# Performance work log

Measured on AMD Instinct MI355X. Metric: run time of the kernel, lower is better.

Reference implementation:

```python
import jax, jax.numpy as jnp
import numpy as np


def setup_inputs() -> dict:
    key = jax.random.key(0)
    ks = jax.random.split(key, 5)
    B, C, H, W = 4, 64, 64, 64
    C8 = C // 8
    return {
        "x_opt": jax.random.normal(ks[0], (B, C, H, W), jnp.float32),
        "x_sar": jax.random.normal(ks[1], (B, C, H, W), jnp.float32),
        "wq": jax.random.normal(ks[2], (C8, C), jnp.float32) * 0.05,
        "bq": jnp.zeros((C8,), jnp.float32),
        "wk": jax.random.normal(ks[3], (C8, C), jnp.float32) * 0.05,
        "bk": jnp.zeros((C8,), jnp.float32),
        "wv": jax.random.normal(ks[4], (C, C), jnp.float32) * 0.05,
        "bv": jnp.zeros((C,), jnp.float32),
        "gamma": jnp.zeros((1,), jnp.float32),
    }


def reference(x_opt, x_sar, wq, bq, wk, bk, wv, bv, gamma):
    b, c, h, w = x_opt.shape
    n = h * w
    xo = x_opt.reshape(b, c, n)  # [b, c, N]
    xs = x_sar.reshape(b, c, n)
    # 1x1 convs == channel matmuls
    q = jnp.einsum('oc,bcn->bon', wq, xo) + bq[None, :, None]  # [b, c//8, N]
    k = jnp.einsum('oc,bcn->bon', wk, xs) + bk[None, :, None]  # [b, c//8, N]
    v = jnp.einsum('oc,bcn->bon', wv, xs) + bv[None, :, None]  # [b, c, N]
    # attn[b, n, m] = softmax_m( q[:, :, n] . k[:, :, m] )  -- NO 1/sqrt(d) scaling
    scores = jnp.einsum('bdn,bdm->bnm', q, k)  # [b, N, N]
    attn = jax.nn.softmax(scores, axis=-1)
    # out[b, c, n] = sum_m v[b, c, m] * attn[b, n, m]
    out = jnp.einsum('bcm,bnm->bcn', v, attn).reshape(b, c, h, w)
    return gamma[0] * out + x_opt
```

## Files before the change

### kernel.cpp

```cpp
#include <hip/hip_runtime.h>
#include <hip/hip_bf16.h>
#include <stdint.h>

#define NDIM 4096
#define CDIM 64
#define NSPLIT 8
#define SPAN (NDIM / NSPLIT)
#define LOG2E 1.44269504088896f

typedef float f32x16 __attribute__((ext_vector_type(16)));
typedef short bf16x8 __attribute__((ext_vector_type(8)));
union U4B { uint4 u; bf16x8 b; };

static __device__ __forceinline__ uint32_t cvtpk(float lo, float hi) {
  uint32_t r;
  asm("v_cvt_pk_bf16_f32 %0, %1, %2" : "=v"(r) : "v"(lo), "v"(hi));
  return r;
}
static __device__ __forceinline__ uint16_t f2bf(float f) {
  uint32_t r;
  asm("v_cvt_pk_bf16_f32 %0, %1, %1" : "=v"(r) : "v"(f));
  return (uint16_t)r;
}
static __device__ __forceinline__ float fexp2(float x) {
  return __builtin_amdgcn_exp2f(x);
}

__global__ __launch_bounds__(256) void proj_kernel(
    const float* __restrict__ x_opt, const float* __restrict__ x_sar,
    const float* __restrict__ wq, const float* __restrict__ bq,
    const float* __restrict__ wk, const float* __restrict__ bk,
    const float* __restrict__ wvp, const float* __restrict__ bv,
    uint16_t* __restrict__ qf, uint16_t* __restrict__ kfp,
    uint16_t* __restrict__ vf2)
{
  const int tid = threadIdx.x;
  const int w = tid >> 6;
  const int l = tid & 63;
  const int x = l & 31;
  const int hi = l >> 5;

  const int id = blockIdx.x;
  const int b = id >> 7;
  const int n0 = (id & 127) * 32;
  const size_t xbase = (size_t)b * CDIM * NDIM;

  const float* xsrc = (w == 2) ? x_opt : x_sar;
  bf16x8 xB[4];
#pragma unroll
  for (int kc = 0; kc < 4; kc++) {
    float sv[8];
#pragma unroll
    for (int j = 0; j < 8; j++)
      sv[j] = xsrc[xbase + (size_t)(kc * 16 + hi * 8 + j) * NDIM + n0 + x];
    U4B us;
    us.u = make_uint4(cvtpk(sv[0], sv[1]), cvtpk(sv[2], sv[3]),
                      cvtpk(sv[4], sv[5]), cvtpk(sv[6], sv[7]));
    xB[kc] = us.b;
  }

  bf16x8 aF[4];
#pragma unroll
  for (int kc = 0; kc < 4; kc++) {
    U4B ua;
    ua.u = make_uint4(0u, 0u, 0u, 0u);
    if (w < 2) {
      const float* wr = wvp + (w * 32 + x) * 64 + kc * 16 + hi * 8;
      float4 wa = ((const float4*)wr)[0];
      float4 wb = ((const float4*)wr)[1];
      ua.u = make_uint4(cvtpk(wa.x, wa.y), cvtpk(wa.z, wa.w),
                        cvtpk(wb.x, wb.y), cvtpk(wb.z, wb.w));
    } else if (x < 8) {
      const float* wr = ((w == 2) ? wq : wk) + x * 64 + kc * 16 + hi * 8;
      float4 wa = ((const float4*)wr)[0];
      float4 wb = ((const float4*)wr)[1];
      ua.u = make_uint4(cvtpk(wa.x, wa.y), cvtpk(wa.z, wa.w),
                        cvtpk(wb.x, wb.y), cvtpk(wb.z, wb.w));
    }
    aF[kc] = ua.b;
  }

  const f32x16 z16 = {0.f,0.f,0.f,0.f, 0.f,0.f,0.f,0.f,
                      0.f,0.f,0.f,0.f, 0.f,0.f,0.f,0.f};
  f32x16 acc = z16;
#pragma unroll
  for (int kc = 0; kc < 4; kc++)
    acc = __builtin_amdgcn_mfma_f32_32x32x16_bf16(aF[kc], xB[kc], acc, 0, 0, 0);

  if (w < 2) {
    const size_t kbbase = (size_t)b * 256 + (n0 >> 4) + (x >> 4);
    const int kk = x & 15;
#pragma unroll
    for (int r = 0; r < 16; r++) {
      const int row = w * 32 + (r & 3) + 8 * (r >> 2) + 4 * hi;
      vf2[(kbbase * 64 + row) * 16 + kk] = f2bf(acc[r] + bv[row]);
    }
  } else if (w == 2) {
    float gv[4];
#pragma unroll
    for (int r = 0; r < 4; r++) gv[r] = (acc[r] + bq[4 * hi + r]) * LOG2E;
    const size_t nrow = ((size_t)b * NDIM + n0 + x) * 16;
    uint2 st;
    st.x = cvtpk(gv[0], gv[1]); st.y = cvtpk(gv[2], gv[3]);
    *(uint2*)(qf + nrow + hi * 4) = st;
    if (hi == 0) {
      const uint4 z4 = make_uint4(0u, 0u, 0u, 0u);
      *(uint4*)(qf + nrow + 8) = z4;
    }
  } else {
    float gv[4];
#pragma unroll
    for (int r = 0; r < 4; r++) gv[r] = acc[r] + bk[4 * hi + r];
    uint2 st;
    st.x = cvtpk(gv[0], gv[1]); st.y = cvtpk(gv[2], gv[3]);
    *(uint2*)(kfp + ((size_t)b * NDIM + n0 + x) * 8 + hi * 4) = st;
  }
}

__global__ __launch_bounds__(256, 4) void attn_kernel(
    const uint16_t* __restrict__ qf, const uint16_t* __restrict__ kfp,
    const uint16_t* __restrict__ vf2,
    uint16_t* __restrict__ po, float* __restrict__ ls)
{
  const int tid = threadIdx.x;
  const int w = tid >> 6;
  const int l = tid & 63;
  const int x = l & 31;
  const int hi = l >> 5;

  const int id = blockIdx.x;
  const int sp = id & 7;
  const int qb = (id >> 3) & 31;
  const int b = id >> 8;

  const int n0 = qb * 128;
  const int qrow = n0 + w * 32 + x;

  U4B qfr;
  qfr.u = *(const uint4*)(qf + ((size_t)b * NDIM + qrow) * 16 + hi * 8);

  const uint32_t hmask = hi ? 0u : 0xFFFFFFFFu;

  const uint16_t* kbase = kfp + ((size_t)b * NDIM + sp * SPAN + x) * 8;
  const uint16_t* vbase =
      vf2 + (((size_t)b * 256 + sp * 32) * 64 + x) * 16 + hi * 8;

  const f32x16 z16 = {0.f,0.f,0.f,0.f, 0.f,0.f,0.f,0.f,
                      0.f,0.f,0.f,0.f, 0.f,0.f,0.f,0.f};
  f32x16 oacc0 = z16, oacc1 = z16;
  float lacc[4] = {0.f, 0.f, 0.f, 0.f};

  uint4 kc   = *(const uint4*)(kbase);
  uint4 va00 = *(const uint4*)(vbase);
  uint4 va01 = *(const uint4*)(vbase + 512);
  uint4 va10 = *(const uint4*)(vbase + 1024);
  uint4 va11 = *(const uint4*)(vbase + 1536);

#pragma unroll
  for (int gq = 0; gq < 16; gq++) {
    const int vo = (gq + 1) * 2048;
    uint4 kn   = *(const uint4*)(kbase + (gq + 1) * 256);
    uint4 vn00 = *(const uint4*)(vbase + vo);
    uint4 vn01 = *(const uint4*)(vbase + vo + 512);
    uint4 vn10 = *(const uint4*)(vbase + vo + 1024);
    uint4 vn11 = *(const uint4*)(vbase + vo + 1536);

    U4B ka;
    ka.u.x = kc.x & hmask; ka.u.y = kc.y & hmask;
    ka.u.z = kc.z & hmask; ka.u.w = kc.w & hmask;
    f32x16 s = __builtin_amdgcn_mfma_f32_32x32x16_bf16(ka.b, qfr.b, z16, 0, 0, 0);

    uint32_t W[8];
#pragma unroll
    for (int j = 0; j < 8; j++) {
      const float p0 = fexp2(s[2 * j]);
      const float p1 = fexp2(s[2 * j + 1]);
      W[j] = cvtpk(p0, p1);
      lacc[j & 3] += p0 + p1;
    }

    __builtin_amdgcn_s_setprio(1);
    {
      uint32_t a0 = W[0], b0 = W[2], a1 = W[1], b1 = W[3];
      asm("v_permlane32_swap_b32 %0, %1" : "+v"(a0), "+v"(b0));
      asm("v_permlane32_swap_b32 %0, %1" : "+v"(a1), "+v"(b1));
      U4B pf, va, vb;
      pf.u = make_uint4(a0, a1, b0, b1);
      va.u = va00; vb.u = va01;
      oacc0 = __builtin_amdgcn_mfma_f32_32x32x16_bf16(va.b, pf.b, oacc0, 0, 0, 0);
      oacc1 = __builtin_amdgcn_mfma_f32_32x32x16_bf16(vb.b, pf.b, oacc1, 0, 0, 0);
    }
    {
      uint32_t a0 = W[4], b0 = W[6], a1 = W[5], b1 = W[7];
      asm("v_permlane32_swap_b32 %0, %1" : "+v"(a0), "+v"(b0));
      asm("v_permlane32_swap_b32 %0, %1" : "+v"(a1), "+v"(b1));
      U4B pf, va, vb;
      pf.u = make_uint4(a0, a1, b0, b1);
      va.u = va10; vb.u = va11;
      oacc0 = __builtin_amdgcn_mfma_f32_32x32x16_bf16(va.b, pf.b, oacc0, 0, 0, 0);
      oacc1 = __builtin_amdgcn_mfma_f32_32x32x16_bf16(vb.b, pf.b, oacc1, 0, 0, 0);
    }
    __builtin_amdgcn_s_setprio(0);

    __builtin_amdgcn_s_barrier();

    kc = kn; va00 = vn00; va01 = vn01; va10 = vn10; va11 = vn11;
  }

  uint16_t* prow = po + (((size_t)sp * 4 + b) * NDIM + qrow) * CDIM;
#pragma unroll
  for (int cb = 0; cb < 2; cb++) {
    const f32x16 oa = (cb == 0) ? oacc0 : oacc1;
#pragma unroll
    for (int u = 0; u < 4; u++) {
      uint2 st;
      st.x = cvtpk(oa[u * 4 + 0], oa[u * 4 + 1]);
      st.y = cvtpk(oa[u * 4 + 2], oa[u * 4 + 3]);
      *(uint2*)(prow + cb * 32 + u * 8 + hi * 4) = st;
    }
  }
  float ltot = (lacc[0] + lacc[1]) + (lacc[2] + lacc[3]);
  ltot += __shfl_xor(ltot, 32);
  if (hi == 0)
    ls[((size_t)sp * 4 + b) * NDIM + qrow] = ltot;
}

__global__ __launch_bounds__(256) void merge_kernel(
    const uint16_t* __restrict__ po, const float* __restrict__ ls,
    const float* __restrict__ x_opt, const float* __restrict__ gamma,
    float* __restrict__ out)
{
  __shared__ float ot[32][65];
  const int tid = threadIdx.x;
  const int b = blockIdx.x >> 7;
  const int n0 = (blockIdx.x & 127) * 32;
  {
    const int q = tid >> 3;
    const int co = (tid & 7) * 8;
    const int nq = n0 + q;
    float wsum = 0.f;
    float acc[8] = {0.f, 0.f, 0.f, 0.f, 0.f, 0.f, 0.f, 0.f};
#pragma unroll
    for (int s = 0; s < NSPLIT; s++) {
      wsum += ls[((size_t)s * 4 + b) * NDIM + nq];
      const uint4 pv = *(const uint4*)(po + (((size_t)s * 4 + b) * NDIM + nq) * CDIM + co);
      const uint32_t* pw = (const uint32_t*)&pv;
#pragma unroll
      for (int j = 0; j < 4; j++) {
        acc[j * 2 + 0] += __uint_as_float(pw[j] << 16);
        acc[j * 2 + 1] += __uint_as_float(pw[j] & 0xFFFF0000u);
      }
    }
    const float inv = 1.f / wsum;
#pragma unroll
    for (int j = 0; j < 8; j++) ot[q][co + j] = acc[j] * inv;
  }
  __syncthreads();
  {
    const float gm = gamma[0];
    const int c = tid >> 2;
    const int j8 = (tid & 3) * 8;
    const float* xp = x_opt + ((size_t)b * CDIM + c) * NDIM + n0 + j8;
    float* op = out + ((size_t)b * CDIM + c) * NDIM + n0 + j8;
#pragma unroll
    for (int h = 0; h < 2; h++) {
      float4 xv = ((const float4*)xp)[h];
      float4 ov;
      ov.x = gm * ot[j8 + h * 4 + 0][c] + xv.x;
      ov.y = gm * ot[j8 + h * 4 + 1][c] + xv.y;
      ov.z = gm * ot[j8 + h * 4 + 2][c] + xv.z;
      ov.w = gm * ot[j8 + h * 4 + 3][c] + xv.w;
      ((float4*)op)[h] = ov;
    }
  }
}

extern "C" void kernel_launch(void* const* d_in, const int* in_sizes, int n_in,
                              void* d_out, int out_size, void* d_ws, size_t ws_size,
                              hipStream_t stream) {
  const float* x_opt = (const float*)d_in[0];
  const float* x_sar = (const float*)d_in[1];
  const float* wq    = (const float*)d_in[2];
  const float* bq    = (const float*)d_in[3];
  const float* wk    = (const float*)d_in[4];
  const float* bk    = (const float*)d_in[5];
  const float* wvp   = (const float*)d_in[6];
  const float* bv    = (const float*)d_in[7];
  const float* gamma = (const float*)d_in[8];
  float* outp = (float*)d_out;

  uint16_t* qf  = (uint16_t*)d_ws;
  uint16_t* kfp = (uint16_t*)((char*)d_ws + 524288);
  uint16_t* vf2 = (uint16_t*)((char*)d_ws + 1048576);
  uint16_t* po  = (uint16_t*)((char*)d_ws + 3145728);
  float* lsp    = (float*)((char*)d_ws + 19922944);

  proj_kernel<<<512, 256, 0, stream>>>(x_opt, x_sar, wq, bq, wk, bk, wvp, bv,
                                       qf, kfp, vf2);
  attn_kernel<<<1024, 256, 0, stream>>>(qf, kfp, vf2, po, lsp);
  merge_kernel<<<512, 256, 0, stream>>>(po, lsp, x_opt, gamma, outp);
}
```

Baseline: 38.66 us.

## Process two query tiles per wave to reuse K/V loads, drop barrier

Each wave now handles 64 query rows (two 32-row MFMA tiles) instead of 32, so every loaded K and V fragment feeds twice as many MFMAs. This halves global/L2 traffic per unit of work and halves the grid to 512 blocks. The per-iteration workgroup barrier is removed and launch bounds drop to 2 waves/SIMD because of doubled accumulator registers. The risks are lower occupancy, less latency hiding, and fewer blocks (512) to fill 256 CUs.

New measurement: 54.93 us. 1.42x slower.

```diff
diff --git a/kernel.cpp b/kernel.cpp
--- a/kernel.cpp
+++ b/kernel.cpp
@@ -117,7 +117,7 @@
   }
 }
 
-__global__ __launch_bounds__(256, 4) void attn_kernel(
+__global__ __launch_bounds__(256, 2) void attn_kernel(
     const uint16_t* __restrict__ qf, const uint16_t* __restrict__ kfp,
     const uint16_t* __restrict__ vf2,
     uint16_t* __restrict__ po, float* __restrict__ ls)
@@ -130,14 +130,15 @@
 
   const int id = blockIdx.x;
   const int sp = id & 7;
-  const int qb = (id >> 3) & 31;
-  const int b = id >> 8;
-
-  const int n0 = qb * 128;
-  const int qrow = n0 + w * 32 + x;
-
-  U4B qfr;
-  qfr.u = *(const uint4*)(qf + ((size_t)b * NDIM + qrow) * 16 + hi * 8);
+  const int qb = (id >> 3) & 15;
+  const int b = id >> 7;
+
+  const int n0 = qb * 256;
+  const int qrow0 = n0 + w * 64 + x;
+
+  U4B qfr0, qfr1;
+  qfr0.u = *(const uint4*)(qf + ((size_t)b * NDIM + qrow0) * 16 + hi * 8);
+  qfr1.u = *(const uint4*)(qf + ((size_t)b * NDIM + qrow0 + 32) * 16 + hi * 8);
 
   const uint32_t hmask = hi ? 0u : 0xFFFFFFFFu;
 
@@ -147,8 +148,10 @@
 
   const f32x16 z16 = {0.f,0.f,0.f,0.f, 0.f,0.f,0.f,0.f,
                       0.f,0.f,0.f,0.f, 0.f,0.f,0.f,0.f};
-  f32x16 oacc0 = z16, oacc1 = z16;
-  float lacc[4] = {0.f, 0.f, 0.f, 0.f};
+  f32x16 oacc00 = z16, oacc01 = z16;
+  f32x16 oacc10 = z16, oacc11 = z16;
+  float lacc0[4] = {0.f, 0.f, 0.f, 0.f};
+  float lacc1[4] = {0.f, 0.f, 0.f, 0.f};
 
   uint4 kc   = *(const uint4*)(kbase);
   uint4 va00 = *(const uint4*)(vbase);
@@ -168,61 +171,82 @@
     U4B ka;
     ka.u.x = kc.x & hmask; ka.u.y = kc.y & hmask;
     ka.u.z = kc.z & hmask; ka.u.w = kc.w & hmask;
-    f32x16 s = __builtin_amdgcn_mfma_f32_32x32x16_bf16(ka.b, qfr.b, z16, 0, 0, 0);
-
-    uint32_t W[8];
+    f32x16 s0 = __builtin_amdgcn_mfma_f32_32x32x16_bf16(ka.b, qfr0.b, z16, 0, 0, 0);
+    f32x16 s1 = __builtin_amdgcn_mfma_f32_32x32x16_bf16(ka.b, qfr1.b, z16, 0, 0, 0);
+
+    uint32_t W0[8], W1[8];
 #pragma unroll
     for (int j = 0; j < 8; j++) {
-      const float p0 = fexp2(s[2 * j]);
-      const float p1 = fexp2(s[2 * j + 1]);
-      W[j] = cvtpk(p0, p1);
-      lacc[j & 3] += p0 + p1;
+      const float a0 = fexp2(s0[2 * j]);
+      const float a1 = fexp2(s0[2 * j + 1]);
+      W0[j] = cvtpk(a0, a1);
+      lacc0[j & 3] += a0 + a1;
+      const float c0 = fexp2(s1[2 * j]);
+      const float c1 = fexp2(s1[2 * j + 1]);
+      W1[j] = cvtpk(c0, c1);
+      lacc1[j & 3] += c0 + c1;
     }
 
     __builtin_amdgcn_s_setprio(1);
     {
-      uint32_t a0 = W[0], b0 = W[2], a1 = W[1], b1 = W[3];
+      uint32_t a0 = W0[0], b0 = W0[2], a1 = W0[1], b1 = W0[3];
+      uint32_t c0 = W1[0], d0 = W1[2], c1 = W1[1], d1 = W1[3];
       asm("v_permlane32_swap_b32 %0, %1" : "+v"(a0), "+v"(b0));
       asm("v_permlane32_swap_b32 %0, %1" : "+v"(a1), "+v"(b1));
-      U4B pf, va, vb;
-      pf.u = make_uint4(a0, a1, b0, b1);
+      asm("v_permlane32_swap_b32 %0, %1" : "+v"(c0), "+v"(d0));
+      asm("v_permlane32_swap_b32 %0, %1" : "+v"(c1), "+v"(d1));
+      U4B pf0, pf1, va, vb;
+      pf0.u = make_uint4(a0, a1, b0, b1);
+      pf1.u = make_uint4(c0, c1, d0, d1);
       va.u = va00; vb.u = va01;
-      oacc0 = __builtin_amdgcn_mfma_f32_32x32x16_bf16(va.b, pf.b, oacc0, 0, 0, 0);
-      oacc1 = __builtin_amdgcn_mfma_f32_32x32x16_bf16(vb.b, pf.b, oacc1, 0, 0, 0);
+      oacc00 = __builtin_amdgcn_mfma_f32_32x32x16_bf16(va.b, pf0.b, oacc00, 0, 0, 0);
+      oacc01 = __builtin_amdgcn_mfma_f32_32x32x16_bf16(vb.b, pf0.b, oacc01, 0, 0, 0);
+      oacc10 = __builtin_amdgcn_mfma_f32_32x32x16_bf16(va.b, pf1.b, oacc10, 0, 0, 0);
+      oacc11 = __builtin_amdgcn_mfma_f32_32x32x16_bf16(vb.b, pf1.b, oacc11, 0, 0, 0);
     }
     {
-      uint32_t a0 = W[4], b0 = W[6], a1 = W[5], b1 = W[7];
+      uint32_t a0 = W0[4], b0 = W0[6], a1 = W0[5], b1 = W0[7];
+      uint32_t c0 = W1[4], d0 = W1[6], c1 = W1[5], d1 = W1[7];
       asm("v_permlane32_swap_b32 %0, %1" : "+v"(a0), "+v"(b0));
       asm("v_permlane32_swap_b32 %0, %1" : "+v"(a1), "+v"(b1));
-      U4B pf, va, vb;
-      pf.u = make_uint4(a0, a1, b0, b1);
+      asm("v_permlane32_swap_b32 %0, %1" : "+v"(c0), "+v"(d0));
+      asm("v_permlane32_swap_b32 %0, %1" : "+v"(c1), "+v"(d1));
+      U4B pf0, pf1, va, vb;
+      pf0.u = make_uint4(a0, a1, b0, b1);
+      pf1.u = make_uint4(c0, c1, d0, d1);
       va.u = va10; vb.u = va11;
-      oacc0 = __builtin_amdgcn_mfma_f32_32x32x16_bf16(va.b, pf.b, oacc0, 0, 0, 0);
-      oacc1 = __builtin_amdgcn_mfma_f32_32x32x16_bf16(vb.b, pf.b, oacc1, 0, 0, 0);
+      oacc00 = __builtin_amdgcn_mfma_f32_32x32x16_bf16(va.b, pf0.b, oacc00, 0, 0, 0);
+      oacc01 = __builtin_amdgcn_mfma_f32_32x32x16_bf16(vb.b, pf0.b, oacc01, 0, 0, 0);
+      oacc10 = __builtin_amdgcn_mfma_f32_32x32x16_bf16(va.b, pf1.b, oacc10, 0, 0, 0);
+      oacc11 = __builtin_amdgcn_mfma_f32_32x32x16_bf16(vb.b, pf1.b, oacc11, 0, 0, 0);
     }
     __builtin_amdgcn_s_setprio(0);
 
-    __builtin_amdgcn_s_barrier();
-
     kc = kn; va00 = vn00; va01 = vn01; va10 = vn10; va11 = vn11;
   }
 
-  uint16_t* prow = po + (((size_t)sp * 4 + b) * NDIM + qrow) * CDIM;
-#pragma unroll
-  for (int cb = 0; cb < 2; cb++) {
-    const f32x16 oa = (cb == 0) ? oacc0 : oacc1;
-#pragma unroll
-    for (int u = 0; u < 4; u++) {
-      uint2 st;
-      st.x = cvtpk(oa[u * 4 + 0], oa[u * 4 + 1]);
-      st.y = cvtpk(oa[u * 4 + 2], oa[u * 4 + 3]);
-      *(uint2*)(prow + cb * 32 + u * 8 + hi * 4) = st;
-    }
-  }
-  float ltot = (lacc[0] + lacc[1]) + (lacc[2] + lacc[3]);
-  ltot += __shfl_xor(ltot, 32);
-  if (hi == 0)
-    ls[((size_t)sp * 4 + b) * NDIM + qrow] = ltot;
+#pragma unroll
+  for (int f = 0; f < 2; f++) {
+    const int qrow = qrow0 + f * 32;
+    uint16_t* prow = po + (((size_t)sp * 4 + b) * NDIM + qrow) * CDIM;
+#pragma unroll
+    for (int cb = 0; cb < 2; cb++) {
+      const f32x16 oa = (f == 0) ? (cb == 0 ? oacc00 : oacc01)
+                                 : (cb == 0 ? oacc10 : oacc11);
+#pragma unroll
+      for (int u = 0; u < 4; u++) {
+        uint2 st;
+        st.x = cvtpk(oa[u * 4 + 0], oa[u * 4 + 1]);
+        st.y = cvtpk(oa[u * 4 + 2], oa[u * 4 + 3]);
+        *(uint2*)(prow + cb * 32 + u * 8 + hi * 4) = st;
+      }
+    }
+    float ltot = (f == 0) ? (lacc0[0] + lacc0[1]) + (lacc0[2] + lacc0[3])
+                          : (lacc1[0] + lacc1[1]) + (lacc1[2] + lacc1[3]);
+    ltot += __shfl_xor(ltot, 32);
+    if (hi == 0)
+      ls[((size_t)sp * 4 + b) * NDIM + qrow] = ltot;
+  }
 }
 
 __global__ __launch_bounds__(256) void merge_kernel(
@@ -297,6 +321,6 @@
 
   proj_kernel<<<512, 256, 0, stream>>>(x_opt, x_sar, wq, bq, wk, bk, wvp, bv,
                                        qf, kfp, vf2);
-  attn_kernel<<<1024, 256, 0, stream>>>(qf, kfp, vf2, po, lsp);
+  attn_kernel<<<512, 256, 0, stream>>>(qf, kfp, vf2, po, lsp);
   merge_kernel<<<512, 256, 0, stream>>>(po, lsp, x_opt, gamma, outp);
 }
```

## Store attention partials channel-major and simplify merge without LDS transpose

Applied to the files above, without the earlier changes.

The attention kernel now writes its per-split partial outputs in a channel-major [split, b*c, N] layout. This lets the merge kernel read partials, softmax sums and x_opt with contiguous vector loads and write the output directly, with no shared-memory transpose or __syncthreads. The change also drops the per-iteration s_barrier and the hi-lane masking of the K operand, which relies on the zero padding of the Q operand to keep the result correct. In exchange, the attention epilogue now issues many scattered 2-byte stores instead of a few 8-byte ones.

New measurement: 36.66 us. 5.2% less time.

```diff
diff --git a/kernel.cpp b/kernel.cpp
--- a/kernel.cpp
+++ b/kernel.cpp
@@ -6,8 +6,10 @@
 #define CDIM 64
 #define NSPLIT 8
 #define SPAN (NDIM / NSPLIT)
+#define NQ4 (SPAN / 32)
 #define LOG2E 1.44269504088896f
 
+typedef float f32x4 __attribute__((ext_vector_type(4)));
 typedef float f32x16 __attribute__((ext_vector_type(16)));
 typedef short bf16x8 __attribute__((ext_vector_type(8)));
 union U4B { uint4 u; bf16x8 b; };
@@ -120,7 +122,7 @@
 __global__ __launch_bounds__(256, 4) void attn_kernel(
     const uint16_t* __restrict__ qf, const uint16_t* __restrict__ kfp,
     const uint16_t* __restrict__ vf2,
-    uint16_t* __restrict__ po, float* __restrict__ ls)
+    uint16_t* __restrict__ po2, float* __restrict__ ls)
 {
   const int tid = threadIdx.x;
   const int w = tid >> 6;
@@ -139,8 +141,6 @@
   U4B qfr;
   qfr.u = *(const uint4*)(qf + ((size_t)b * NDIM + qrow) * 16 + hi * 8);
 
-  const uint32_t hmask = hi ? 0u : 0xFFFFFFFFu;
-
   const uint16_t* kbase = kfp + ((size_t)b * NDIM + sp * SPAN + x) * 8;
   const uint16_t* vbase =
       vf2 + (((size_t)b * 256 + sp * 32) * 64 + x) * 16 + hi * 8;
@@ -157,7 +157,7 @@
   uint4 va11 = *(const uint4*)(vbase + 1536);
 
 #pragma unroll
-  for (int gq = 0; gq < 16; gq++) {
+  for (int gq = 0; gq < NQ4; gq++) {
     const int vo = (gq + 1) * 2048;
     uint4 kn   = *(const uint4*)(kbase + (gq + 1) * 256);
     uint4 vn00 = *(const uint4*)(vbase + vo);
@@ -165,9 +165,7 @@
     uint4 vn10 = *(const uint4*)(vbase + vo + 1024);
     uint4 vn11 = *(const uint4*)(vbase + vo + 1536);
 
-    U4B ka;
-    ka.u.x = kc.x & hmask; ka.u.y = kc.y & hmask;
-    ka.u.z = kc.z & hmask; ka.u.w = kc.w & hmask;
+    U4B ka; ka.u = kc;
     f32x16 s = __builtin_amdgcn_mfma_f32_32x32x16_bf16(ka.b, qfr.b, z16, 0, 0, 0);
 
     uint32_t W[8];
@@ -202,21 +200,16 @@
     }
     __builtin_amdgcn_s_setprio(0);
 
-    __builtin_amdgcn_s_barrier();
-
     kc = kn; va00 = vn00; va01 = vn01; va10 = vn10; va11 = vn11;
   }
 
-  uint16_t* prow = po + (((size_t)sp * 4 + b) * NDIM + qrow) * CDIM;
-#pragma unroll
-  for (int cb = 0; cb < 2; cb++) {
-    const f32x16 oa = (cb == 0) ? oacc0 : oacc1;
-#pragma unroll
-    for (int u = 0; u < 4; u++) {
-      uint2 st;
-      st.x = cvtpk(oa[u * 4 + 0], oa[u * 4 + 1]);
-      st.y = cvtpk(oa[u * 4 + 2], oa[u * 4 + 3]);
-      *(uint2*)(prow + cb * 32 + u * 8 + hi * 4) = st;
+  {
+    uint16_t* pb = po2 + ((size_t)(sp * 256 + b * 64 + hi * 4)) * NDIM + qrow;
+#pragma unroll
+    for (int r = 0; r < 16; r++) {
+      const size_t off = (size_t)((r & 3) + 8 * (r >> 2)) * NDIM;
+      pb[off] = f2bf(oacc0[r]);
+      pb[off + (size_t)32 * NDIM] = f2bf(oacc1[r]);
     }
   }
   float ltot = (lacc[0] + lacc[1]) + (lacc[2] + lacc[3]);
@@ -226,53 +219,47 @@
 }
 
 __global__ __launch_bounds__(256) void merge_kernel(
-    const uint16_t* __restrict__ po, const float* __restrict__ ls,
+    const uint16_t* __restrict__ po2, const float* __restrict__ ls,
     const float* __restrict__ x_opt, const float* __restrict__ gamma,
     float* __restrict__ out)
 {
-  __shared__ float ot[32][65];
-  const int tid = threadIdx.x;
-  const int b = blockIdx.x >> 7;
-  const int n0 = (blockIdx.x & 127) * 32;
-  {
-    const int q = tid >> 3;
-    const int co = (tid & 7) * 8;
-    const int nq = n0 + q;
-    float wsum = 0.f;
-    float acc[8] = {0.f, 0.f, 0.f, 0.f, 0.f, 0.f, 0.f, 0.f};
-#pragma unroll
-    for (int s = 0; s < NSPLIT; s++) {
-      wsum += ls[((size_t)s * 4 + b) * NDIM + nq];
-      const uint4 pv = *(const uint4*)(po + (((size_t)s * 4 + b) * NDIM + nq) * CDIM + co);
-      const uint32_t* pw = (const uint32_t*)&pv;
-#pragma unroll
-      for (int j = 0; j < 4; j++) {
-        acc[j * 2 + 0] += __uint_as_float(pw[j] << 16);
-        acc[j * 2 + 1] += __uint_as_float(pw[j] & 0xFFFF0000u);
-      }
-    }
-    const float inv = 1.f / wsum;
-#pragma unroll
-    for (int j = 0; j < 8; j++) ot[q][co + j] = acc[j] * inv;
-  }
-  __syncthreads();
-  {
-    const float gm = gamma[0];
-    const int c = tid >> 2;
-    const int j8 = (tid & 3) * 8;
-    const float* xp = x_opt + ((size_t)b * CDIM + c) * NDIM + n0 + j8;
-    float* op = out + ((size_t)b * CDIM + c) * NDIM + n0 + j8;
-#pragma unroll
-    for (int h = 0; h < 2; h++) {
-      float4 xv = ((const float4*)xp)[h];
-      float4 ov;
-      ov.x = gm * ot[j8 + h * 4 + 0][c] + xv.x;
-      ov.y = gm * ot[j8 + h * 4 + 1][c] + xv.y;
-      ov.z = gm * ot[j8 + h * 4 + 2][c] + xv.z;
-      ov.w = gm * ot[j8 + h * 4 + 3][c] + xv.w;
-      ((float4*)op)[h] = ov;
-    }
-  }
+  const int idx = blockIdx.x * 256 + threadIdx.x;
+  const int n8 = (idx & 511) << 3;
+  const int row = idx >> 9;
+  const int b = row >> 6;
+
+  float acc[8] = {0.f, 0.f, 0.f, 0.f, 0.f, 0.f, 0.f, 0.f};
+  f32x4 ws0 = {0.f, 0.f, 0.f, 0.f};
+  f32x4 ws1 = {0.f, 0.f, 0.f, 0.f};
+#pragma unroll
+  for (int s = 0; s < NSPLIT; s++) {
+    const uint4 pv = *(const uint4*)(po2 + ((size_t)s * 256 + row) * NDIM + n8);
+    const uint32_t* pw = (const uint32_t*)&pv;
+#pragma unroll
+    for (int j = 0; j < 4; j++) {
+      acc[j * 2 + 0] += __uint_as_float(pw[j] << 16);
+      acc[j * 2 + 1] += __uint_as_float(pw[j] & 0xFFFF0000u);
+    }
+    const float* lp = ls + ((size_t)s * 4 + b) * NDIM + n8;
+    ws0 += *(const f32x4*)(lp);
+    ws1 += *(const f32x4*)(lp + 4);
+  }
+  const float gm = gamma[0];
+  const float* xp = x_opt + (size_t)row * NDIM + n8;
+  float* op = out + (size_t)row * NDIM + n8;
+  float4 x0 = ((const float4*)xp)[0];
+  float4 x1 = ((const float4*)xp)[1];
+  float4 o0, o1;
+  o0.x = gm * acc[0] / ws0[0] + x0.x;
+  o0.y = gm * acc[1] / ws0[1] + x0.y;
+  o0.z = gm * acc[2] / ws0[2] + x0.z;
+  o0.w = gm * acc[3] / ws0[3] + x0.w;
+  o1.x = gm * acc[4] / ws1[0] + x1.x;
+  o1.y = gm * acc[5] / ws1[1] + x1.y;
+  o1.z = gm * acc[6] / ws1[2] + x1.z;
+  o1.w = gm * acc[7] / ws1[3] + x1.w;
+  ((float4*)op)[0] = o0;
+  ((float4*)op)[1] = o1;
 }
 
 extern "C" void kernel_launch(void* const* d_in, const int* in_sizes, int n_in,
@@ -292,11 +279,11 @@
   uint16_t* qf  = (uint16_t*)d_ws;
   uint16_t* kfp = (uint16_t*)((char*)d_ws + 524288);
   uint16_t* vf2 = (uint16_t*)((char*)d_ws + 1048576);
-  uint16_t* po  = (uint16_t*)((char*)d_ws + 3145728);
+  uint16_t* po2 = (uint16_t*)((char*)d_ws + 3145728);
   float* lsp    = (float*)((char*)d_ws + 19922944);
 
   proj_kernel<<<512, 256, 0, stream>>>(x_opt, x_sar, wq, bq, wk, bk, wvp, bv,
                                        qf, kfp, vf2);
-  attn_kernel<<<1024, 256, 0, stream>>>(qf, kfp, vf2, po, lsp);
-  merge_kernel<<<512, 256, 0, stream>>>(po, lsp, x_opt, gamma, outp);
-}
+  attn_kernel<<<1024, 256, 0, stream>>>(qf, kfp, vf2, po2, lsp);
+  merge_kernel<<<512, 256, 0, stream>>>(po2, lsp, x_opt, gamma, outp);
+}
```
